# Kernel tuning notes

Hardware: AMD Instinct MI355X
Metric: run time of the kernel (lower is better)

## Reference

```python
import jax, jax.numpy as jnp
import numpy as np

B = 4096
DIM = 2048
B1 = 25   # root children (level-2 inner nodes)
B2 = 40   # leaves per level-2 node
NUM_CLASSES = B1 * B2  # 1000


def setup_inputs() -> dict:
    key = jax.random.key(0)
    k1, k2, k3, k4 = jax.random.split(key, 4)
    x = jax.random.normal(k1, (B, DIM), dtype=jnp.float32)
    labels = jax.random.randint(k2, (B,), 0, NUM_CLASSES, dtype=jnp.int64)
    # per-node Linear(dim, num_child + 1); column 0 = 'not in subtree'
    W_root = jax.random.normal(k3, (DIM, B1 + 1), dtype=jnp.float32) * 0.02
    b_root = jnp.zeros((B1 + 1,), dtype=jnp.float32)
    W_lvl2 = jax.random.normal(k4, (B1, DIM, B2 + 1), dtype=jnp.float32) * 0.02
    b_lvl2 = jnp.zeros((B1, B2 + 1), dtype=jnp.float32)
    return {"x": x, "labels": labels, "W_root": W_root, "b_root": b_root,
            "W_lvl2": W_lvl2, "b_lvl2": b_lvl2}


def reference(x, labels, W_root, b_root, W_lvl2, b_lvl2):
    b = x.shape[0]
    b1 = W_lvl2.shape[0]
    b2 = W_lvl2.shape[2] - 1

    # layer 1: root classifier (root.path_prob == 1.0)
    root_logits = x @ W_root + b_root                       # [B, b1+1]
    root_lp = jax.nn.log_softmax(root_logits, axis=-1)
    root_prob = jnp.exp(root_lp)

    # layer 2: all level-2 node classifiers as one grouped GEMM
    lvl2_logits = jnp.einsum('bd,ndk->bnk', x, W_lvl2) + b_lvl2  # [B, b1, b2+1]
    lvl2_lp = jax.nn.log_softmax(lvl2_logits, axis=-1)
    lvl2_prob = jnp.exp(lvl2_lp)

    # leaf path_prob = P(child under node n) * P(node n under root);
    # leaves tile out columns contiguously (label2id of complete tree)
    out = (lvl2_prob[:, :, 1:] * root_prob[:, 1:, None]).reshape(b, b1 * b2)

    # penalty: CE at each inner node divided by its layer l
    j = labels // b2                                        # level-2 parent index
    i = labels % b2                                         # leaf index within parent
    ce_root = -jnp.take_along_axis(root_lp, (j + 1)[:, None], axis=1).mean()
    # sub-label for node n: i+1 if label's parent is n, else 0
    sub_lab = jnp.where(j[:, None] == jnp.arange(b1)[None, :], (i + 1)[:, None], 0)
    gathered = jnp.take_along_axis(lvl2_lp, sub_lab[:, :, None], axis=2)[..., 0]  # [B, b1]
    penalty = ce_root + (-gathered).mean(axis=0).sum() / 2.0

    return out, penalty
```

## Files before the change

### kernel.cpp

```cpp
#include <hip/hip_runtime.h>
#include <stdint.h>

#define TB 256

typedef __bf16 bf16x8 __attribute__((ext_vector_type(8)));
typedef float f32x4 __attribute__((ext_vector_type(4)));

#define AS1 __attribute__((address_space(1)))
#define AS3 __attribute__((address_space(3)))
#define GLOAD16(gp, lp) __builtin_amdgcn_global_load_lds( \
    (const AS1 unsigned int*)(gp), (AS3 unsigned int*)(lp), 16, 0, 0)

__device__ __forceinline__ unsigned short f2bf(float f) {
  uint32_t u = __builtin_bit_cast(uint32_t, f);
  u += 0x7fffu + ((u >> 16) & 1u);
  return (unsigned short)(u >> 16);
}

__device__ __forceinline__ void waitbar6() {
  __builtin_amdgcn_sched_barrier(0);
  asm volatile("s_waitcnt vmcnt(6) lgkmcnt(0)" ::: "memory");
  __builtin_amdgcn_s_barrier();
  __builtin_amdgcn_sched_barrier(0);
}
__device__ __forceinline__ void waitbar3() {
  __builtin_amdgcn_sched_barrier(0);
  asm volatile("s_waitcnt vmcnt(3) lgkmcnt(0)" ::: "memory");
  __builtin_amdgcn_s_barrier();
  __builtin_amdgcn_sched_barrier(0);
}
__device__ __forceinline__ void waitbar0() {
  __builtin_amdgcn_sched_barrier(0);
  asm volatile("s_waitcnt vmcnt(0) lgkmcnt(0)" ::: "memory");
  __builtin_amdgcn_s_barrier();
  __builtin_amdgcn_sched_barrier(0);
}

__global__ __launch_bounds__(TB) void k_prep(const float* __restrict__ x,
                                             const float* __restrict__ wl,
                                             const float* __restrict__ wr,
                                             const int* __restrict__ labraw,
                                             unsigned short* __restrict__ xbf,
                                             unsigned short* __restrict__ wlt,
                                             unsigned short* __restrict__ wrt,
                                             int* __restrict__ lab32,
                                             float* __restrict__ pengl) {
  int bid = blockIdx.x, t = threadIdx.x;
  if (bid < 4096) {
    int idx = bid * TB + t;
    const float4* xin = reinterpret_cast<const float4*>(x);
    float4 a = xin[idx * 2], b = xin[idx * 2 + 1];
    uint32_t p0 = f2bf(a.x) | ((uint32_t)f2bf(a.y) << 16);
    uint32_t p1 = f2bf(a.z) | ((uint32_t)f2bf(a.w) << 16);
    uint32_t p2 = f2bf(b.x) | ((uint32_t)f2bf(b.y) << 16);
    uint32_t p3 = f2bf(b.z) | ((uint32_t)f2bf(b.w) << 16);
    reinterpret_cast<uint4*>(xbf)[idx] = make_uint4(p0, p1, p2, p3);
  } else if (bid < 4928) {
    __shared__ float ld_f[2624];
    int b2 = bid - 4096;
    if (b2 < 800) {
      int n = b2 / 32, dt = b2 % 32, d0 = dt * 64;
      const float* src = wl + ((size_t)n * 2048 + d0) * 41;
      for (int i = 0; i < 11; i++) { int lin = t + TB * i; if (lin < 2624) ld_f[lin] = src[lin]; }
      __syncthreads();
      unsigned short* dst = wlt + (size_t)n * 64 * 2048 + d0;
      for (int i = 0; i < 12; i++) {
        int lin = t + TB * i;
        int wc = lin >> 6, d = lin & 63;
        float v = (wc < 41) ? ld_f[d * 41 + wc] : 0.f;
        dst[(size_t)wc * 2048 + d] = f2bf(v);
      }
    } else {
      int dt = b2 - 800, d0 = dt * 64;
      const float* src = wr + (size_t)d0 * 26;
      for (int i = 0; i < 7; i++) { int lin = t + TB * i; if (lin < 1664) ld_f[lin] = src[lin]; }
      __syncthreads();
      unsigned short* dst = wrt + d0;
      for (int i = 0; i < 8; i++) {
        int lin = t + TB * i;
        int wc = lin >> 6, d = lin & 63;
        float v = (wc < 26) ? ld_f[d * 26 + wc] : 0.f;
        dst[(size_t)wc * 2048 + d] = f2bf(v);
      }
    }
  } else {
    __shared__ int orred;
    if (t == 0) { orred = 0; pengl[0] = 0.f; }
    __syncthreads();
    int acc = 0;
    for (int i = t; i < 2048; i += TB) acc |= labraw[2 * i + 1];
    atomicOr(&orred, acc);
    __syncthreads();
    bool i64 = (orred == 0);
    for (int i = t; i < 4096; i += TB) lab32[i] = i64 ? labraw[2 * i] : labraw[i];
  }
}

__global__ __launch_bounds__(TB) void k_root(const unsigned short* __restrict__ xbf,
                                             const unsigned short* __restrict__ wrt,
                                             const float* __restrict__ br,
                                             const int* __restrict__ labels,
                                             float* __restrict__ rootp,
                                             float* __restrict__ pengl) {
  __shared__ __align__(16) unsigned char lds3[3][12288];
  int r0 = blockIdx.x * 64;
  int tid = threadIdx.x, lane = tid & 63, wave = tid >> 6;
  int wavebase = wave * 64;
  int lq = lane >> 4, lr = lane & 15;
  const unsigned short* xg = xbf + (size_t)r0 * 2048;
  f32x4 acc[2] = {};

#define STAGE_RT(lb, kk)                                                              \
  do {                                                                                \
    _Pragma("unroll")                                                                 \
    for (int i = 0; i < 2; i++) {                                                     \
      int c = i * 256 + tid;                                                          \
      int row = c >> 3, s = c & 7;                                                    \
      const unsigned short* gp = xg + (size_t)row * 2048 + (kk) + ((s ^ (row & 7)) << 3); \
      GLOAD16(gp, (lb) + (size_t)(i * 256 + wavebase) * 16);                          \
    }                                                                                 \
    {                                                                                 \
      int wc = tid >> 3, s = tid & 7;                                                 \
      const unsigned short* gp = wrt + (size_t)wc * 2048 + (kk) + ((s ^ (wc & 7)) << 3); \
      GLOAD16(gp, (lb) + 8192 + (size_t)wavebase * 16);                               \
    }                                                                                 \
  } while (0)

#define COMPUTE_RT(base)                                                              \
  do {                                                                                \
    _Pragma("unroll")                                                                 \
    for (int ks = 0; ks < 2; ks++) {                                                  \
      bf16x8 af[2], bx;                                                               \
      _Pragma("unroll")                                                               \
      for (int mt = 0; mt < 2; mt++) {                                                \
        int wc = mt * 16 + lr;                                                        \
        af[mt] = *reinterpret_cast<const bf16x8*>((base) + 8192 + wc * 128 + ((((ks << 2) | lq) ^ (wc & 7)) << 4)); \
      }                                                                               \
      {                                                                               \
        int row = wavebase / 4 + lr;                                \
        bx = *reinterpret_cast<const bf16x8*>((base) + row * 128 + ((((ks << 2) | lq) ^ (row & 7)) << 4)); \
      }                                                                               \
      _Pragma("unroll")                                                               \
      for (int mt = 0; mt < 2; mt++)                                                  \
        acc[mt] = __builtin_amdgcn_mfma_f32_16x16x32_bf16(af[mt], bx, acc[mt], 0, 0, 0); \
    }                                                                                 \
  } while (0)

  STAGE_RT(&lds3[0][0], 0);
  STAGE_RT(&lds3[1][0], 64);
  waitbar3();
  int cur = 0;
#pragma unroll 3
  for (int t = 0; t < 30; ++t) {
    int nx = cur + 2; if (nx >= 3) nx -= 3;
    STAGE_RT(&lds3[nx][0], (t + 2) * 64);
    COMPUTE_RT(&lds3[cur][0]);
    waitbar3();
    ++cur; if (cur == 3) cur = 0;
  }
  COMPUTE_RT(&lds3[cur][0]);
  waitbar0();
  ++cur; if (cur == 3) cur = 0;
  COMPUTE_RT(&lds3[cur][0]);

  float bb[2][4];
#pragma unroll
  for (int mt = 0; mt < 2; mt++)
#pragma unroll
    for (int r = 0; r < 4; r++) {
      int wc = mt * 16 + lq * 4 + r;
      bb[mt][r] = (wc < 26) ? br[wc] : -1e30f;
    }
  int b = r0 + wave * 16 + lr;
  float lg[2][4];
  float m = -1e30f;
#pragma unroll
  for (int mt = 0; mt < 2; mt++)
#pragma unroll
    for (int r = 0; r < 4; r++) {
      float v = acc[mt][r] + bb[mt][r];
      lg[mt][r] = v;
      m = fmaxf(m, v);
    }
  m = fmaxf(m, __shfl_xor(m, 16));
  m = fmaxf(m, __shfl_xor(m, 32));
  float s = 0.f;
#pragma unroll
  for (int mt = 0; mt < 2; mt++)
#pragma unroll
    for (int r = 0; r < 4; r++) s += expf(lg[mt][r] - m);
  s += __shfl_xor(s, 16);
  s += __shfl_xor(s, 32);
  float ls = logf(s);
  int lab = labels[b];
  int j = lab / 40;
  float pen = 0.f;
#pragma unroll
  for (int mt = 0; mt < 2; mt++)
#pragma unroll
    for (int r = 0; r < 4; r++) {
      int wc = mt * 16 + lq * 4 + r;
      float lp = lg[mt][r] - m - ls;
      if (wc < 26) rootp[(size_t)b * 32 + wc] = expf(lp);
      if (wc == j + 1) pen -= lp;
    }
  for (int off = 32; off; off >>= 1) pen += __shfl_down(pen, off);
  float* red = (float*)&lds3[0][0];
  if (lane == 0) red[wave] = pen;
  __syncthreads();
  if (tid == 0) atomicAdd(pengl, (red[0] + red[1] + red[2] + red[3]) * (1.f / 4096.f));
}

__global__ __launch_bounds__(TB) void k_lvl2(const unsigned short* __restrict__ xbf,
                                             const unsigned short* __restrict__ wlt,
                                             const float* __restrict__ bl,
                                             const int* __restrict__ labels,
                                             const float* __restrict__ rootp,
                                             float* __restrict__ out,
                                             float* __restrict__ pengl) {
  __shared__ __align__(16) unsigned char lds3[3][24576];
  int bid = blockIdx.x;
  int swz = (bid & 7) * 100 + (bid >> 3);
  int rt = swz / 25, n = swz % 25;
  int r0 = rt * 128;
  int tid = threadIdx.x, lane = tid & 63, wave = tid >> 6;
  int wavebase = wave * 64;
  int lq = lane >> 4, lr = lane & 15;
  f32x4 acc[3][2] = {};
  const unsigned short* xg = xbf + (size_t)r0 * 2048;
  const unsigned short* wg = wlt + (size_t)n * 64 * 2048;

#define STAGE_L2(lb, kk)                                                              \
  do {                                                                                \
    _Pragma("unroll")                                                                 \
    for (int i = 0; i < 4; i++) {                                                     \
      int c = i * 256 + tid;                                                          \
      int row = c >> 3, s = c & 7;                                                    \
      const unsigned short* gp = xg + (size_t)row * 2048 + (kk) + ((s ^ (row & 7)) << 3); \
      GLOAD16(gp, (lb) + (size_t)(i * 256 + wavebase) * 16);                          \
    }                                                                                 \
    _Pragma("unroll")                                                                 \
    for (int i = 0; i < 2; i++) {                                                     \
      int c = i * 256 + tid;                                                          \
      int wc = c >> 3, s = c & 7;                                                     \
      const unsigned short* gp = wg + (size_t)wc * 2048 + (kk) + ((s ^ (wc & 7)) << 3); \
      GLOAD16(gp, (lb) + 16384 + (size_t)(i * 256 + wavebase) * 16);                  \
    }                                                                                 \
  } while (0)

#define COMPUTE_L2(base)                                                              \
  do {                                                                                \
    _Pragma("unroll")                                                                 \
    for (int ks = 0; ks < 2; ks++) {                                                  \
      bf16x8 af[3], bx[2];                                                            \
      _Pragma("unroll")                                                               \
      for (int mt = 0; mt < 3; mt++) {                                                \
        int wc = mt * 16 + lr;                                                        \
        af[mt] = *reinterpret_cast<const bf16x8*>((base) + 16384 + wc * 128 + ((((ks << 2) | lq) ^ (wc & 7)) << 4)); \
      }                                                                               \
      _Pragma("unroll")                                                               \
      for (int nt = 0; nt < 2; nt++) {                                                \
        int row = wave * 32 + nt * 16 + lr;                                           \
        bx[nt] = *reinterpret_cast<const bf16x8*>((base) + row * 128 + ((((ks << 2) | lq) ^ (row & 7)) << 4)); \
      }                                                                               \
      _Pragma("unroll")                                                               \
      for (int mt = 0; mt < 3; mt++)                                                  \
        _Pragma("unroll")                                                             \
        for (int nt = 0; nt < 2; nt++)                                                \
          acc[mt][nt] = __builtin_amdgcn_mfma_f32_16x16x32_bf16(af[mt], bx[nt], acc[mt][nt], 0, 0, 0); \
    }                                                                                 \
  } while (0)

  STAGE_L2(&lds3[0][0], 0);
  STAGE_L2(&lds3[1][0], 64);
  waitbar6();
  int cur = 0;
#pragma unroll 3
  for (int t = 0; t < 30; ++t) {
    int nx = cur + 2; if (nx >= 3) nx -= 3;
    STAGE_L2(&lds3[nx][0], (t + 2) * 64);
    COMPUTE_L2(&lds3[cur][0]);
    waitbar6();
    ++cur; if (cur == 3) cur = 0;
  }
  COMPUTE_L2(&lds3[cur][0]);
  waitbar0();
  ++cur; if (cur == 3) cur = 0;
  COMPUTE_L2(&lds3[cur][0]);

  float bb[3][4];
#pragma unroll
  for (int mt = 0; mt < 3; mt++)
#pragma unroll
    for (int r = 0; r < 4; r++) {
      int wc = mt * 16 + lq * 4 + r;
      bb[mt][r] = (wc < 41) ? bl[n * 41 + wc] : -1e30f;
    }
  float pen = 0.f;
#pragma unroll
  for (int nt = 0; nt < 2; nt++) {
    int b = r0 + wave * 32 + nt * 16 + lr;
    float lg[3][4];
    float m = -1e30f;
#pragma unroll
    for (int mt = 0; mt < 3; mt++)
#pragma unroll
      for (int r = 0; r < 4; r++) {
        float v = acc[mt][nt][r] + bb[mt][r];
        lg[mt][r] = v;
        m = fmaxf(m, v);
      }
    m = fmaxf(m, __shfl_xor(m, 16));
    m = fmaxf(m, __shfl_xor(m, 32));
    float s = 0.f;
#pragma unroll
    for (int mt = 0; mt < 3; mt++)
#pragma unroll
      for (int r = 0; r < 4; r++) s += expf(lg[mt][r] - m);
    s += __shfl_xor(s, 16);
    s += __shfl_xor(s, 32);
    float ls = logf(s);
    float rp = rootp[(size_t)b * 32 + (n + 1)];
    int lab = labels[b];
    int j = lab / 40;
    int sub = (j == n) ? (lab - j * 40 + 1) : 0;
#pragma unroll
    for (int mt = 0; mt < 3; mt++)
#pragma unroll
      for (int r = 0; r < 4; r++) {
        int wc = mt * 16 + lq * 4 + r;
        float lp = lg[mt][r] - m - ls;
        if (wc >= 1 && wc < 41) out[(size_t)b * 1000 + n * 40 + wc - 1] = expf(lp) * rp;
        if (wc == sub) pen -= lp;
      }
  }
  for (int off = 32; off; off >>= 1) pen += __shfl_down(pen, off);
  float* red = (float*)&lds3[0][0];
  if (lane == 0) red[wave] = pen;
  __syncthreads();
  if (tid == 0) atomicAdd(pengl, (red[0] + red[1] + red[2] + red[3]) * (1.f / 8192.f));
}

extern "C" void kernel_launch(void* const* d_in, const int* in_sizes, int n_in,
                              void* d_out, int out_size, void* d_ws, size_t ws_size,
                              hipStream_t stream) {
  const float* x = (const float*)d_in[0];
  const int* labels_raw = (const int*)d_in[1];
  const float* wroot = (const float*)d_in[2];
  const float* broot = (const float*)d_in[3];
  const float* wlvl2 = (const float*)d_in[4];
  const float* blvl2 = (const float*)d_in[5];
  float* out = (float*)d_out;
  float* pengl = out + 4096000;

  char* ws = (char*)d_ws;
  unsigned short* xbf = (unsigned short*)ws;
  unsigned short* wlt = (unsigned short*)(ws + 16777216);
  unsigned short* wrt = (unsigned short*)(ws + 16777216 + 6553600);
  float* rootp = (float*)(ws + 16777216 + 6553600 + 131072);
  int* lab32 = (int*)(ws + 16777216 + 6553600 + 131072 + 524288);

  k_prep<<<4929, TB, 0, stream>>>(x, wlvl2, wroot, labels_raw, xbf, wlt, wrt, lab32, pengl);
  k_root<<<64, TB, 0, stream>>>(xbf, wrt, broot, lab32, rootp, pengl);
  k_lvl2<<<800, TB, 0, stream>>>(xbf, wlt, blvl2, lab32, rootp, out, pengl);
}
```

Before: 152.8 us.

## Pack node weights to 48 columns, pair nodes per lvl2 block, split-K root GEMM

The level-2 weights are packed to 48 columns per node instead of 64, and each lvl2 block now computes two nodes for 128 rows. This halves the grid, cuts padded MFMA work and reuses each x tile across two nodes, with double buffering replacing triple buffering. The root GEMM now uses 256 blocks of 16 rows with an 8-way split-K across waves, reduced through LDS, to raise parallelism in that small kernel. The changes add an extra prep block to zero the padded 26th node slot, and the fully synchronous double-buffer wait may expose more load latency.

```diff
diff --git a/kernel.cpp b/kernel.cpp
--- a/kernel.cpp
+++ b/kernel.cpp
@@ -17,12 +17,6 @@
   return (unsigned short)(u >> 16);
 }
 
-__device__ __forceinline__ void waitbar6() {
-  __builtin_amdgcn_sched_barrier(0);
-  asm volatile("s_waitcnt vmcnt(6) lgkmcnt(0)" ::: "memory");
-  __builtin_amdgcn_s_barrier();
-  __builtin_amdgcn_sched_barrier(0);
-}
 __device__ __forceinline__ void waitbar3() {
   __builtin_amdgcn_sched_barrier(0);
   asm volatile("s_waitcnt vmcnt(3) lgkmcnt(0)" ::: "memory");
@@ -63,7 +57,7 @@
       const float* src = wl + ((size_t)n * 2048 + d0) * 41;
       for (int i = 0; i < 11; i++) { int lin = t + TB * i; if (lin < 2624) ld_f[lin] = src[lin]; }
       __syncthreads();
-      unsigned short* dst = wlt + (size_t)n * 64 * 2048 + d0;
+      unsigned short* dst = wlt + (size_t)n * 48 * 2048 + d0;
       for (int i = 0; i < 12; i++) {
         int lin = t + TB * i;
         int wc = lin >> 6, d = lin & 63;
@@ -83,7 +77,7 @@
         dst[(size_t)wc * 2048 + d] = f2bf(v);
       }
     }
-  } else {
+  } else if (bid == 4928) {
     __shared__ int orred;
     if (t == 0) { orred = 0; pengl[0] = 0.f; }
     __syncthreads();
@@ -93,67 +87,65 @@
     __syncthreads();
     bool i64 = (orred == 0);
     for (int i = t; i < 4096; i += TB) lab32[i] = i64 ? labraw[2 * i] : labraw[i];
-  }
-}
-
-__global__ __launch_bounds__(TB) void k_root(const unsigned short* __restrict__ xbf,
-                                             const unsigned short* __restrict__ wrt,
-                                             const float* __restrict__ br,
-                                             const int* __restrict__ labels,
-                                             float* __restrict__ rootp,
-                                             float* __restrict__ pengl) {
-  __shared__ __align__(16) unsigned char lds3[3][12288];
-  int r0 = blockIdx.x * 64;
+  } else {
+    uint4* p = reinterpret_cast<uint4*>(wlt + (size_t)25 * 48 * 2048);
+    uint4 z = make_uint4(0, 0, 0, 0);
+    for (int i = t; i < 12288; i += TB) p[i] = z;
+  }
+}
+
+__global__ __launch_bounds__(512) void k_root(const unsigned short* __restrict__ xbf,
+                                              const unsigned short* __restrict__ wrt,
+                                              const float* __restrict__ br,
+                                              const int* __restrict__ labels,
+                                              float* __restrict__ rootp,
+                                              float* __restrict__ pengl) {
+  __shared__ __align__(16) unsigned char lds3[3][24576];
+  int r0 = blockIdx.x * 16;
   int tid = threadIdx.x, lane = tid & 63, wave = tid >> 6;
-  int wavebase = wave * 64;
   int lq = lane >> 4, lr = lane & 15;
   const unsigned short* xg = xbf + (size_t)r0 * 2048;
   f32x4 acc[2] = {};
 
 #define STAGE_RT(lb, kk)                                                              \
   do {                                                                                \
-    _Pragma("unroll")                                                                 \
-    for (int i = 0; i < 2; i++) {                                                     \
-      int c = i * 256 + tid;                                                          \
-      int row = c >> 3, s = c & 7;                                                    \
-      const unsigned short* gp = xg + (size_t)row * 2048 + (kk) + ((s ^ (row & 7)) << 3); \
-      GLOAD16(gp, (lb) + (size_t)(i * 256 + wavebase) * 16);                          \
-    }                                                                                 \
-    {                                                                                 \
-      int wc = tid >> 3, s = tid & 7;                                                 \
-      const unsigned short* gp = wrt + (size_t)wc * 2048 + (kk) + ((s ^ (wc & 7)) << 3); \
-      GLOAD16(gp, (lb) + 8192 + (size_t)wavebase * 16);                               \
+    {                                                    \
+      int row = tid >> 5, s = tid & 31;                                               \
+      const unsigned short* gp = xg + (size_t)row * 2048 + (kk) + ((s ^ row) << 3);   \
+      GLOAD16(gp, (lb) + (size_t)tid * 16);                                           \
+    }                                                                                 \
+    _Pragma("unroll")                                                                 \
+    for (int i = 0; i < 2; i++) {                       \
+      int idx = i * 512 + tid;                                                        \
+      int wc = idx >> 5, s = idx & 31;                                                \
+      const unsigned short* gp = wrt + (size_t)wc * 2048 + (kk) + ((s ^ (wc & 31)) << 3); \
+      GLOAD16(gp, (lb) + 8192 + (size_t)idx * 16);                                    \
     }                                                                                 \
   } while (0)
 
 #define COMPUTE_RT(base)                                                              \
   do {                                                                                \
-    _Pragma("unroll")                                                                 \
-    for (int ks = 0; ks < 2; ks++) {                                                  \
-      bf16x8 af[2], bx;                                                               \
-      _Pragma("unroll")                                                               \
-      for (int mt = 0; mt < 2; mt++) {                                                \
-        int wc = mt * 16 + lr;                                                        \
-        af[mt] = *reinterpret_cast<const bf16x8*>((base) + 8192 + wc * 128 + ((((ks << 2) | lq) ^ (wc & 7)) << 4)); \
-      }                                                                               \
-      {                                                                               \
-        int row = wavebase / 4 + lr;                                \
-        bx = *reinterpret_cast<const bf16x8*>((base) + row * 128 + ((((ks << 2) | lq) ^ (row & 7)) << 4)); \
-      }                                                                               \
-      _Pragma("unroll")                                                               \
-      for (int mt = 0; mt < 2; mt++)                                                  \
-        acc[mt] = __builtin_amdgcn_mfma_f32_16x16x32_bf16(af[mt], bx, acc[mt], 0, 0, 0); \
-    }                                                                                 \
+    int g = (wave << 2) | lq;                      \
+    bf16x8 af[2], bx;                                                                 \
+    _Pragma("unroll")                                                                 \
+    for (int mt = 0; mt < 2; mt++) {                                                  \
+      int c = mt * 16 + lr;                                                           \
+      af[mt] = *reinterpret_cast<const bf16x8*>((base) + 8192 + c * 512 + ((g ^ (c & 31)) << 4)); \
+    }                                                                                 \
+    bx = *reinterpret_cast<const bf16x8*>((base) + lr * 512 + ((g ^ lr) << 4));       \
+    _Pragma("unroll")                                                                 \
+    for (int mt = 0; mt < 2; mt++)                                                    \
+      acc[mt] = __builtin_amdgcn_mfma_f32_16x16x32_bf16(af[mt], bx, acc[mt], 0, 0, 0); \
   } while (0)
 
   STAGE_RT(&lds3[0][0], 0);
-  STAGE_RT(&lds3[1][0], 64);
+  STAGE_RT(&lds3[1][0], 256);
   waitbar3();
   int cur = 0;
 #pragma unroll 3
-  for (int t = 0; t < 30; ++t) {
+  for (int t = 0; t < 6; ++t) {
     int nx = cur + 2; if (nx >= 3) nx -= 3;
-    STAGE_RT(&lds3[nx][0], (t + 2) * 64);
+    STAGE_RT(&lds3[nx][0], (t + 2) * 256);
     COMPUTE_RT(&lds3[cur][0]);
     waitbar3();
     ++cur; if (cur == 3) cur = 0;
@@ -162,53 +154,56 @@
   waitbar0();
   ++cur; if (cur == 3) cur = 0;
   COMPUTE_RT(&lds3[cur][0]);
-
-  float bb[2][4];
+  __syncthreads();
+
+  float* red = (float*)&lds3[0][0];
+  int li = (wave * 64 + lane) * 8;
 #pragma unroll
   for (int mt = 0; mt < 2; mt++)
 #pragma unroll
-    for (int r = 0; r < 4; r++) {
-      int wc = mt * 16 + lq * 4 + r;
-      bb[mt][r] = (wc < 26) ? br[wc] : -1e30f;
-    }
-  int b = r0 + wave * 16 + lr;
-  float lg[2][4];
-  float m = -1e30f;
-#pragma unroll
-  for (int mt = 0; mt < 2; mt++)
-#pragma unroll
-    for (int r = 0; r < 4; r++) {
-      float v = acc[mt][r] + bb[mt][r];
-      lg[mt][r] = v;
-      m = fmaxf(m, v);
-    }
-  m = fmaxf(m, __shfl_xor(m, 16));
-  m = fmaxf(m, __shfl_xor(m, 32));
-  float s = 0.f;
-#pragma unroll
-  for (int mt = 0; mt < 2; mt++)
-#pragma unroll
-    for (int r = 0; r < 4; r++) s += expf(lg[mt][r] - m);
-  s += __shfl_xor(s, 16);
-  s += __shfl_xor(s, 32);
-  float ls = logf(s);
-  int lab = labels[b];
-  int j = lab / 40;
-  float pen = 0.f;
-#pragma unroll
-  for (int mt = 0; mt < 2; mt++)
-#pragma unroll
-    for (int r = 0; r < 4; r++) {
-      int wc = mt * 16 + lq * 4 + r;
-      float lp = lg[mt][r] - m - ls;
-      if (wc < 26) rootp[(size_t)b * 32 + wc] = expf(lp);
-      if (wc == j + 1) pen -= lp;
-    }
-  for (int off = 32; off; off >>= 1) pen += __shfl_down(pen, off);
-  float* red = (float*)&lds3[0][0];
-  if (lane == 0) red[wave] = pen;
+    for (int r = 0; r < 4; r++) red[li + mt * 4 + r] = acc[mt][r];
   __syncthreads();
-  if (tid == 0) atomicAdd(pengl, (red[0] + red[1] + red[2] + red[3]) * (1.f / 4096.f));
+  if (wave == 0) {
+    float lg[2][4];
+    float m = -1e30f;
+#pragma unroll
+    for (int mt = 0; mt < 2; mt++)
+#pragma unroll
+      for (int r = 0; r < 4; r++) {
+        float v = 0.f;
+#pragma unroll
+        for (int w = 0; w < 8; w++) v += red[(w * 64 + lane) * 8 + mt * 4 + r];
+        int wc = mt * 16 + lq * 4 + r;
+        v += (wc < 26) ? br[wc] : -1e30f;
+        lg[mt][r] = v;
+        m = fmaxf(m, v);
+      }
+    m = fmaxf(m, __shfl_xor(m, 16));
+    m = fmaxf(m, __shfl_xor(m, 32));
+    float s = 0.f;
+#pragma unroll
+    for (int mt = 0; mt < 2; mt++)
+#pragma unroll
+      for (int r = 0; r < 4; r++) s += expf(lg[mt][r] - m);
+    s += __shfl_xor(s, 16);
+    s += __shfl_xor(s, 32);
+    float ls = logf(s);
+    int b = r0 + lr;
+    int lab = labels[b];
+    int j = lab / 40;
+    float pen = 0.f;
+#pragma unroll
+    for (int mt = 0; mt < 2; mt++)
+#pragma unroll
+      for (int r = 0; r < 4; r++) {
+        int wc = mt * 16 + lq * 4 + r;
+        float lp = lg[mt][r] - m - ls;
+        if (wc < 26) rootp[(size_t)b * 32 + wc] = expf(lp);
+        if (wc == j + 1) pen -= lp;
+      }
+    for (int off = 32; off; off >>= 1) pen += __shfl_down(pen, off);
+    if (lane == 0) atomicAdd(pengl, pen * (1.f / 4096.f));
+  }
 }
 
 __global__ __launch_bounds__(TB) void k_lvl2(const unsigned short* __restrict__ xbf,
@@ -218,33 +213,33 @@
                                              const float* __restrict__ rootp,
                                              float* __restrict__ out,
                                              float* __restrict__ pengl) {
-  __shared__ __align__(16) unsigned char lds3[3][24576];
+  __shared__ __align__(16) unsigned char ldsb[2][28672];
   int bid = blockIdx.x;
-  int swz = (bid & 7) * 100 + (bid >> 3);
-  int rt = swz / 25, n = swz % 25;
-  int r0 = rt * 128;
+  int swz = (bid & 7) * 52 + (bid >> 3);
+  int rt = swz / 13, gp = swz % 13;
+  int r0 = rt * 128, n0 = gp * 2;
   int tid = threadIdx.x, lane = tid & 63, wave = tid >> 6;
-  int wavebase = wave * 64;
+  int wr = wave >> 1, wcq = wave & 1;
   int lq = lane >> 4, lr = lane & 15;
-  f32x4 acc[3][2] = {};
+  f32x4 acc[3][4] = {};
   const unsigned short* xg = xbf + (size_t)r0 * 2048;
-  const unsigned short* wg = wlt + (size_t)n * 64 * 2048;
+  const unsigned short* wg = wlt + (size_t)n0 * 48 * 2048;
 
 #define STAGE_L2(lb, kk)                                                              \
   do {                                                                                \
     _Pragma("unroll")                                                                 \
-    for (int i = 0; i < 4; i++) {                                                     \
-      int c = i * 256 + tid;                                                          \
-      int row = c >> 3, s = c & 7;                                                    \
+    for (int i = 0; i < 4; i++) {                                 \
+      int idx = i * 256 + tid;                                                        \
+      int row = idx >> 3, s = idx & 7;                                                \
       const unsigned short* gp = xg + (size_t)row * 2048 + (kk) + ((s ^ (row & 7)) << 3); \
-      GLOAD16(gp, (lb) + (size_t)(i * 256 + wavebase) * 16);                          \
-    }                                                                                 \
-    _Pragma("unroll")                                                                 \
-    for (int i = 0; i < 2; i++) {                                                     \
-      int c = i * 256 + tid;                                                          \
-      int wc = c >> 3, s = c & 7;                                                     \
+      GLOAD16(gp, (lb) + (size_t)idx * 16);                                           \
+    }                                                                                 \
+    _Pragma("unroll")                                                                 \
+    for (int i = 0; i < 3; i++) {                        \
+      int idx = i * 256 + tid;                                                        \
+      int wc = idx >> 3, s = idx & 7;                                                 \
       const unsigned short* gp = wg + (size_t)wc * 2048 + (kk) + ((s ^ (wc & 7)) << 3); \
-      GLOAD16(gp, (lb) + 16384 + (size_t)(i * 256 + wavebase) * 16);                  \
+      GLOAD16(gp, (lb) + 16384 + (size_t)idx * 16);                                   \
     }                                                                                 \
   } while (0)
 
@@ -252,54 +247,49 @@
   do {                                                                                \
     _Pragma("unroll")                                                                 \
     for (int ks = 0; ks < 2; ks++) {                                                  \
-      bf16x8 af[3], bx[2];                                                            \
+      int g = (ks << 2) | lq;                                                         \
+      bf16x8 af[3], bx[4];                                                            \
       _Pragma("unroll")                                                               \
       for (int mt = 0; mt < 3; mt++) {                                                \
-        int wc = mt * 16 + lr;                                                        \
-        af[mt] = *reinterpret_cast<const bf16x8*>((base) + 16384 + wc * 128 + ((((ks << 2) | lq) ^ (wc & 7)) << 4)); \
+        int c = wcq * 48 + mt * 16 + lr;                                              \
+        af[mt] = *reinterpret_cast<const bf16x8*>((base) + 16384 + c * 128 + ((g ^ (c & 7)) << 4)); \
       }                                                                               \
       _Pragma("unroll")                                                               \
-      for (int nt = 0; nt < 2; nt++) {                                                \
-        int row = wave * 32 + nt * 16 + lr;                                           \
-        bx[nt] = *reinterpret_cast<const bf16x8*>((base) + row * 128 + ((((ks << 2) | lq) ^ (row & 7)) << 4)); \
+      for (int nt = 0; nt < 4; nt++) {                                                \
+        int row = wr * 64 + nt * 16 + lr;                                             \
+        bx[nt] = *reinterpret_cast<const bf16x8*>((base) + row * 128 + ((g ^ (row & 7)) << 4)); \
       }                                                                               \
       _Pragma("unroll")                                                               \
       for (int mt = 0; mt < 3; mt++)                                                  \
         _Pragma("unroll")                                                             \
-        for (int nt = 0; nt < 2; nt++)                                                \
+        for (int nt = 0; nt < 4; nt++)                                                \
           acc[mt][nt] = __builtin_amdgcn_mfma_f32_16x16x32_bf16(af[mt], bx[nt], acc[mt][nt], 0, 0, 0); \
     }                                                                                 \
   } while (0)
 
-  STAGE_L2(&lds3[0][0], 0);
-  STAGE_L2(&lds3[1][0], 64);
-  waitbar6();
-  int cur = 0;
-#pragma unroll 3
-  for (int t = 0; t < 30; ++t) {
-    int nx = cur + 2; if (nx >= 3) nx -= 3;
-    STAGE_L2(&lds3[nx][0], (t + 2) * 64);
-    COMPUTE_L2(&lds3[cur][0]);
-    waitbar6();
-    ++cur; if (cur == 3) cur = 0;
-  }
-  COMPUTE_L2(&lds3[cur][0]);
+  STAGE_L2(&ldsb[0][0], 0);
   waitbar0();
-  ++cur; if (cur == 3) cur = 0;
-  COMPUTE_L2(&lds3[cur][0]);
-
+#pragma unroll 2
+  for (int t = 0; t < 32; ++t) {
+    if (t < 31) STAGE_L2(&ldsb[(t + 1) & 1][0], (t + 1) * 64);
+    COMPUTE_L2(&ldsb[t & 1][0]);
+    waitbar0();
+  }
+
+  int n = n0 + wcq;
+  bool valid = (n < 25);
   float bb[3][4];
 #pragma unroll
   for (int mt = 0; mt < 3; mt++)
 #pragma unroll
     for (int r = 0; r < 4; r++) {
-      int wc = mt * 16 + lq * 4 + r;
-      bb[mt][r] = (wc < 41) ? bl[n * 41 + wc] : -1e30f;
+      int wcg = mt * 16 + lq * 4 + r;
+      bb[mt][r] = (valid && wcg < 41) ? bl[n * 41 + wcg] : -1e30f;
     }
   float pen = 0.f;
 #pragma unroll
-  for (int nt = 0; nt < 2; nt++) {
-    int b = r0 + wave * 32 + nt * 16 + lr;
+  for (int nt = 0; nt < 4; nt++) {
+    int b = r0 + wr * 64 + nt * 16 + lr;
     float lg[3][4];
     float m = -1e30f;
 #pragma unroll
@@ -320,7 +310,7 @@
     s += __shfl_xor(s, 16);
     s += __shfl_xor(s, 32);
     float ls = logf(s);
-    float rp = rootp[(size_t)b * 32 + (n + 1)];
+    float rp = valid ? rootp[(size_t)b * 32 + (n + 1)] : 0.f;
     int lab = labels[b];
     int j = lab / 40;
     int sub = (j == n) ? (lab - j * 40 + 1) : 0;
@@ -328,14 +318,14 @@
     for (int mt = 0; mt < 3; mt++)
 #pragma unroll
       for (int r = 0; r < 4; r++) {
-        int wc = mt * 16 + lq * 4 + r;
+        int wcg = mt * 16 + lq * 4 + r;
         float lp = lg[mt][r] - m - ls;
-        if (wc >= 1 && wc < 41) out[(size_t)b * 1000 + n * 40 + wc - 1] = expf(lp) * rp;
-        if (wc == sub) pen -= lp;
+        if (valid && wcg >= 1 && wcg < 41) out[(size_t)b * 1000 + n * 40 + wcg - 1] = expf(lp) * rp;
+        if (valid && wcg == sub) pen -= lp;
       }
   }
   for (int off = 32; off; off >>= 1) pen += __shfl_down(pen, off);
-  float* red = (float*)&lds3[0][0];
+  float* red = (float*)&ldsb[0][0];
   if (lane == 0) red[wave] = pen;
   __syncthreads();
   if (tid == 0) atomicAdd(pengl, (red[0] + red[1] + red[2] + red[3]) * (1.f / 8192.f));
@@ -356,11 +346,11 @@
   char* ws = (char*)d_ws;
   unsigned short* xbf = (unsigned short*)ws;
   unsigned short* wlt = (unsigned short*)(ws + 16777216);
-  unsigned short* wrt = (unsigned short*)(ws + 16777216 + 6553600);
-  float* rootp = (float*)(ws + 16777216 + 6553600 + 131072);
-  int* lab32 = (int*)(ws + 16777216 + 6553600 + 131072 + 524288);
-
-  k_prep<<<4929, TB, 0, stream>>>(x, wlvl2, wroot, labels_raw, xbf, wlt, wrt, lab32, pengl);
-  k_root<<<64, TB, 0, stream>>>(xbf, wrt, broot, lab32, rootp, pengl);
-  k_lvl2<<<800, TB, 0, stream>>>(xbf, wlt, blvl2, lab32, rootp, out, pengl);
-}
+  unsigned short* wrt = (unsigned short*)(ws + 21889024);
+  float* rootp = (float*)(ws + 22020096);
+  int* lab32 = (int*)(ws + 22544384);
+
+  k_prep<<<4930, TB, 0, stream>>>(x, wlvl2, wroot, labels_raw, xbf, wlt, wrt, lab32, pengl);
+  k_root<<<256, 512, 0, stream>>>(xbf, wrt, broot, lab32, rootp, pengl);
+  k_lvl2<<<416, TB, 0, stream>>>(xbf, wlt, blvl2, lab32, rootp, out, pengl);
+}
```

Result: faster. 147.3 us (-3.6%).
